# Performance work log

Hardware: AMD Instinct MI355X
Metric: run time of the kernel (lower is better)

## Reference

```python
import jax, jax.numpy as jnp
import numpy as np

ROOT_2 = 1.41421
C = 256
DIV = 4
CP = C // DIV  # 64


def _spectral_normalize(w2d):
    # exact largest singular value (torch uses power iteration approx of this)
    s = jnp.linalg.norm(w2d, ord=2)
    return w2d / s


def setup_inputs() -> dict:
    key = jax.random.key(0)
    ks = jax.random.split(key, 10)
    B, H, W = 8, 64, 64
    x = jax.random.normal(ks[0], (B, C, H, W), dtype=jnp.float32)
    # 1x1 conv weights stored as [out, in]; spectral-normalized like torch's spectral_norm
    def conv_w(k, o, i):
        w = jax.random.normal(k, (o, i), dtype=jnp.float32) * (1.0 / np.sqrt(i))
        return _spectral_normalize(w)
    Wq = conv_w(ks[1], CP, C); bq = jnp.zeros((CP,), jnp.float32)
    Wk = conv_w(ks[2], CP, C); bk = jnp.zeros((CP,), jnp.float32)
    Wv = conv_w(ks[3], CP, C); bv = jnp.zeros((CP,), jnp.float32)
    Wo = conv_w(ks[4], C, CP); bo = jnp.zeros((C,), jnp.float32)
    gamma = jnp.zeros((1,), jnp.float32)
    return {"x": x, "Wq": Wq, "bq": bq, "Wk": Wk, "bk": bk,
            "Wv": Wv, "bv": bv, "Wo": Wo, "bo": bo, "gamma": gamma}


def reference(x, Wq, bq, Wk, bk, Wv, bv, Wo, bo, gamma):
    B, c, h, w = x.shape
    n = h * w
    const1 = jnp.float32(ROOT_2 / np.sqrt(C))       # Weight_Scaling(in_channels)
    const2 = jnp.float32(ROOT_2 / np.sqrt(CP))      # Weight_Scaling(in_channels//div_num)
    xs = (const1 * x).reshape(B, c, n)              # [B,C,N]
    q = jnp.einsum('oc,bcn->bon', Wq, xs) + bq[None, :, None]  # [B,C',N]
    k = jnp.einsum('oc,bcn->bon', Wk, xs) + bk[None, :, None]
    v = jnp.einsum('oc,bcn->bon', Wv, xs) + bv[None, :, None]
    # attn[b,i,j] = softmax_j(q[:,i]^T k[:,j])
    scores = jnp.einsum('bcn,bcm->bnm', q, k)       # [B,N,N]
    attn = jax.nn.softmax(scores, axis=-1)
    sa = jnp.einsum('bcm,bnm->bcn', v, attn)        # v @ attn^T
    sa = const2 * sa
    out = jnp.einsum('oc,bcn->bon', Wo, sa) + bo[None, :, None]  # [B,C,N]
    out = out.reshape(B, c, h, w)
    return gamma[0] * out + x
```

## Files before the change

### kernel.cpp

```cpp
#include <hip/hip_runtime.h>


#define Bsz 8
#define Cch 256
#define CPd 64
#define Nn  4096
#define TIL 64
#define NSPL 4
#define MQUAR (Nn / NSPL)

typedef __attribute__((ext_vector_type(8))) short short8;
typedef __attribute__((ext_vector_type(4))) float f32x4;

static constexpr float C1 = (float)(1.41421 / 16.0);
static constexpr float C2 = (float)(1.41421 / 8.0);

__device__ inline unsigned pk_trunc(float lo, float hi) {
    return __builtin_amdgcn_perm(__float_as_uint(hi), __float_as_uint(lo), 0x07060302u);
}
__device__ inline float dpp_swap1(float v) {
    return __uint_as_float((unsigned)__builtin_amdgcn_mov_dpp(
        (int)__float_as_uint(v), 0xB1, 0xF, 0xF, true));
}
__device__ __forceinline__ void gl16(const unsigned short* g, unsigned short* s) {
    __builtin_amdgcn_global_load_lds(
        (const __attribute__((address_space(1))) void*)g,
        (__attribute__((address_space(3))) void*)s, 16, 0, 0);
}

__global__ __launch_bounds__(256) void wconv_kernel(
    const float* __restrict__ Wq, const float* __restrict__ Wk,
    const float* __restrict__ Wv, const float* __restrict__ Wo,
    unsigned short* __restrict__ Wb)
{
    const int idx = (blockIdx.x * 256 + threadIdx.x) * 4;
    const float* src = (idx < 16384) ? Wq : (idx < 32768) ? Wk : (idx < 49152) ? Wv : Wo;
    const float4 v = *(const float4*)(src + (idx & 16383));
    *(uint2*)(Wb + idx) = make_uint2(pk_trunc(v.x, v.y), pk_trunc(v.z, v.w));
}

__global__ __launch_bounds__(256) void qkv_kernel(
    const float* __restrict__ x, const unsigned short* __restrict__ Wb,
    const float* __restrict__ bq, const float* __restrict__ bk, const float* __restrict__ bv,
    unsigned short* __restrict__ qT, unsigned short* __restrict__ kT,
    unsigned short* __restrict__ vB)
{
    __shared__ __align__(16) unsigned short Wlds[CPd * 264];
    __shared__ __align__(16) float T[TIL * 68];

    const int b   = blockIdx.y;
    const int n0  = blockIdx.x * TIL;
    const int t   = threadIdx.x;
    const int g   = t >> 6;
    const int l15 = t & 15;
    const int l4  = (t & 63) >> 4;

    const float* xb = x + (size_t)b * Cch * Nn + n0 + 16 * g + l15;
    short8 xf[8];
    #pragma unroll
    for (int ks = 0; ks < 8; ++ks) {
        float xr[8];
        #pragma unroll
        for (int j = 0; j < 8; ++j)
            xr[j] = C1 * xb[(size_t)(8 * l4 + 32 * ks + j) * Nn];
        union { unsigned u[4]; short8 s; } p;
        p.u[0] = pk_trunc(xr[0], xr[1]); p.u[1] = pk_trunc(xr[2], xr[3]);
        p.u[2] = pk_trunc(xr[4], xr[5]); p.u[3] = pk_trunc(xr[6], xr[7]);
        xf[ks] = p.s;
    }

    #pragma unroll
    for (int mat = 0; mat < 3; ++mat) {
        {
            const uint4* wg = (const uint4*)(Wb + mat * 16384);
            #pragma unroll
            for (int p = 0; p < 8; ++p) {
                const int idx = p * 256 + t;
                const int o = idx >> 5, cs = idx & 31;
                *(uint4*)&Wlds[o * 264 + cs * 8] = wg[idx];
            }
        }
        __syncthreads();

        const float* bias = (mat == 0) ? bq : (mat == 1) ? bk : bv;
        f32x4 acc[4];
        #pragma unroll
        for (int st = 0; st < 4; ++st) {
            const float bb = bias[16 * st + l15];
            acc[st] = (f32x4){bb, bb, bb, bb};
        }
        #pragma unroll
        for (int st = 0; st < 4; ++st) {
            #pragma unroll
            for (int ks = 0; ks < 8; ++ks) {
                const short8 wf = *(const short8*)&Wlds[(16 * st + l15) * 264 + 8 * l4 + 32 * ks];
                acc[st] = __builtin_amdgcn_mfma_f32_16x16x32_bf16(xf[ks], wf, acc[st], 0, 0, 0);
            }
        }
        __syncthreads();

        if (mat < 2) {
            #pragma unroll
            for (int st = 0; st < 4; ++st)
                #pragma unroll
                for (int r = 0; r < 4; ++r)
                    T[(16 * g + 4 * l4 + r) * 68 + 16 * st + l15] = acc[st][r];
        } else {
            #pragma unroll
            for (int st = 0; st < 4; ++st)
                #pragma unroll
                for (int r = 0; r < 4; ++r)
                    T[(16 * st + l15) * 68 + 16 * g + 4 * l4 + r] = acc[st][r];
        }
        __syncthreads();

        const int row = t >> 2;
        const int sg  = 16 * (t & 3);
        const float4 a0 = *(const float4*)&T[row * 68 + sg + 0];
        const float4 a1 = *(const float4*)&T[row * 68 + sg + 4];
        const float4 a2 = *(const float4*)&T[row * 68 + sg + 8];
        const float4 a3 = *(const float4*)&T[row * 68 + sg + 12];
        const uint4 lo = make_uint4(pk_trunc(a0.x, a0.y), pk_trunc(a0.z, a0.w),
                                    pk_trunc(a1.x, a1.y), pk_trunc(a1.z, a1.w));
        const uint4 hi = make_uint4(pk_trunc(a2.x, a2.y), pk_trunc(a2.z, a2.w),
                                    pk_trunc(a3.x, a3.y), pk_trunc(a3.z, a3.w));
        unsigned short* dst;
        if (mat < 2) {
            dst = (mat == 0 ? qT : kT) + ((size_t)(b * Nn + n0 + row)) * CPd + sg;
        } else {
            dst = vB + ((size_t)(b * CPd + row)) * Nn + n0 + sg;
        }
        *(uint4*)dst = lo;
        *(uint4*)(dst + 8) = hi;
    }
}

__global__ __launch_bounds__(256, 6) void flash_kernel(
    const unsigned short* __restrict__ qT, const unsigned short* __restrict__ kT,
    const unsigned short* __restrict__ vB, float* __restrict__ Op, float* __restrict__ Lg)
{
    __shared__ __align__(16) unsigned short Ks[TIL * 64];
    __shared__ __align__(16) unsigned short Vs[TIL * 64];
    __shared__ __align__(16) unsigned Pb[TIL * 34];
    __shared__ float Lsh[TIL];

    const int b   = blockIdx.y;
    const int n0  = blockIdx.x * TIL;
    const int s   = blockIdx.z;
    const int t   = threadIdx.x;
    const int l   = t & 63;
    const int g   = t >> 6;
    const int l15 = l & 15;
    const int l4  = l >> 4;
    const int par = l & 1;
    const unsigned sel = par ? 0x03020706u : 0x07060302u;
    const int l15h = l15 >> 1;

    if (t < TIL) Lsh[t] = 0.f;

    const unsigned short* qp = qT + (size_t)(b * Nn + n0 + 16 * g + l15) * CPd + 8 * l4;
    const short8 qf0 = *(const short8*)qp;
    const short8 qf1 = *(const short8*)(qp + 32);

    f32x4 acco[4];
    #pragma unroll
    for (int ct = 0; ct < 4; ++ct) acco[ct] = (f32x4){0.f, 0.f, 0.f, 0.f};
    float Lp[4] = {0.f, 0.f, 0.f, 0.f};

    const int r16 = (l >> 3) & 7;
    const int sch = (l & 7) ^ r16;
    const unsigned short* kSrc = kT + (size_t)b * Nn * CPd
                               + (size_t)(16 * g + r16) * CPd + sch * 8;
    const unsigned short* vSrc = vB + (size_t)b * CPd * Nn
                               + (size_t)(16 * g + r16) * Nn + sch * 8;
    unsigned short* KsW = &Ks[(16 * g) * 64];
    unsigned short* VsW = &Vs[(16 * g) * 64];

    const int h7  = l15 & 7;
    const int sw0 = (l4 ^ h7) << 4;
    const char* KsB = (const char*)Ks + (l15 << 7);
    const char* VsB = (const char*)Vs + (l15 << 7);

    const int mbase = s * MQUAR;
    for (int mi = 0; mi < MQUAR; mi += TIL) {
        const int m0 = mbase + mi;
        __syncthreads();
        gl16(kSrc + (size_t)m0 * CPd,       KsW);
        gl16(kSrc + (size_t)(m0 + 8) * CPd, KsW + 8 * 64);
        gl16(vSrc + m0,                     VsW);
        gl16(vSrc + (size_t)8 * Nn + m0,    VsW + 8 * 64);
        __syncthreads();

        f32x4 accs[4];
        #pragma unroll
        for (int st = 0; st < 4; ++st) {
            accs[st] = (f32x4){0.f, 0.f, 0.f, 0.f};
            const short8 kf0 = *(const short8*)(KsB + (st << 11) + sw0);
            const short8 kf1 = *(const short8*)(KsB + (st << 11) + (sw0 ^ 64));
            accs[st] = __builtin_amdgcn_mfma_f32_16x16x32_bf16(qf0, kf0, accs[st], 0, 0, 0);
            accs[st] = __builtin_amdgcn_mfma_f32_16x16x32_bf16(qf1, kf1, accs[st], 0, 0, 0);
        }

        #pragma unroll
        for (int st = 0; st < 4; ++st) {
            unsigned u[4];
            #pragma unroll
            for (int r = 0; r < 4; ++r) {
                float p = __expf(accs[st][r]);
                Lp[r] += p;
                float nb = dpp_swap1(p);
                u[r] = __builtin_amdgcn_perm(__float_as_uint(nb), __float_as_uint(p), sel);
            }
            const int rb = 16 * g + 4 * l4 + 2 * par;
            Pb[(rb + 0) * 34 + 8 * st + l15h] = u[2 * par];
            Pb[(rb + 1) * 34 + 8 * st + l15h] = u[2 * par + 1];
        }
        __syncthreads();

        #pragma unroll
        for (int ks = 0; ks < 2; ++ks) {
            const short8 pf = *(const short8*)&Pb[(16 * g + l15) * 34 + 4 * l4 + 16 * ks];
            const int swk = sw0 ^ (ks << 6);
            #pragma unroll
            for (int ct = 0; ct < 4; ++ct) {
                const short8 vf = *(const short8*)(VsB + (ct << 11) + swk);
                acco[ct] = __builtin_amdgcn_mfma_f32_16x16x32_bf16(pf, vf, acco[ct], 0, 0, 0);
            }
        }
    }

    #pragma unroll
    for (int r = 0; r < 4; ++r) atomicAdd(&Lsh[16 * g + 4 * l4 + r], Lp[r]);
    __syncthreads();

    float* ob = Op + ((size_t)(b * Nn + n0)) * CPd;
    #pragma unroll
    for (int r = 0; r < 4; ++r) {
        const int nl = 16 * g + 4 * l4 + r;
        #pragma unroll
        for (int ct = 0; ct < 4; ++ct)
            atomicAdd(&ob[(size_t)nl * CPd + 16 * ct + l15], acco[ct][r]);
    }
    if (t < TIL) atomicAdd(&Lg[(size_t)b * Nn + n0 + t], Lsh[t]);
}

__global__ __launch_bounds__(512) void out_kernel(
    const float* __restrict__ Op, const float* __restrict__ Lg,
    const unsigned short* __restrict__ Wob,
    const float* __restrict__ bo, const float* __restrict__ gamma,
    const float* __restrict__ x, float* __restrict__ y)
{
    __shared__ __align__(16) unsigned short Wos[Cch * 72];
    __shared__ __align__(16) unsigned short Sas[TIL * 72];
    __shared__ float bos[Cch];

    const int b   = blockIdx.y;
    const int n0  = blockIdx.x * TIL;
    const int t   = threadIdx.x;
    const int l   = t & 63;
    const int w   = t >> 6;
    const int l15 = l & 15;
    const int l4  = l >> 4;

    if (t < Cch) bos[t] = bo[t];
    {
        const uint4* wg = (const uint4*)Wob;
        #pragma unroll
        for (int p = 0; p < 4; ++p) {
            const int idx = p * 512 + t;
            const int row = idx >> 3, seg = idx & 7;
            *(uint4*)&Wos[row * 72 + seg * 8] = wg[idx];
        }
    }
    if (t < 256) {
        const int n = t >> 2, seg = t & 3;
        const float* o0 = Op + ((size_t)(b * Nn + n0 + n)) * CPd + seg * 16;
        const float sc = C2 / Lg[(size_t)b * Nn + n0 + n];
        unsigned pk[8];
        #pragma unroll
        for (int i = 0; i < 4; ++i) {
            const float4 a = ((const float4*)o0)[i];
            pk[2 * i]     = pk_trunc(a.x * sc, a.y * sc);
            pk[2 * i + 1] = pk_trunc(a.z * sc, a.w * sc);
        }
        *(uint4*)&Sas[n * 72 + seg * 16]     = make_uint4(pk[0], pk[1], pk[2], pk[3]);
        *(uint4*)&Sas[n * 72 + seg * 16 + 8] = make_uint4(pk[4], pk[5], pk[6], pk[7]);
    }
    __syncthreads();

    short8 bfr[4][2];
    #pragma unroll
    for (int ns = 0; ns < 4; ++ns) {
        bfr[ns][0] = *(const short8*)&Sas[(16 * ns + l15) * 72 + 8 * l4];
        bfr[ns][1] = *(const short8*)&Sas[(16 * ns + l15) * 72 + 8 * l4 + 32];
    }
    const float gam = gamma[0];
    const float* xb = x + (size_t)b * Cch * Nn;
    float*       yb = y + (size_t)b * Cch * Nn;

    #pragma unroll
    for (int os2 = 0; os2 < 2; ++os2) {
        const int obase = 16 * (w + 8 * os2);
        const short8 af0 = *(const short8*)&Wos[(obase + l15) * 72 + 8 * l4];
        const short8 af1 = *(const short8*)&Wos[(obase + l15) * 72 + 8 * l4 + 32];
        #pragma unroll
        for (int ns = 0; ns < 4; ++ns) {
            f32x4 acc = (f32x4){0.f, 0.f, 0.f, 0.f};
            acc = __builtin_amdgcn_mfma_f32_16x16x32_bf16(af0, bfr[ns][0], acc, 0, 0, 0);
            acc = __builtin_amdgcn_mfma_f32_16x16x32_bf16(af1, bfr[ns][1], acc, 0, 0, 0);
            #pragma unroll
            for (int r = 0; r < 4; ++r) {
                const int o = obase + 4 * l4 + r;
                const size_t idx = (size_t)o * Nn + n0 + 16 * ns + l15;
                yb[idx] = fmaf(gam, acc[r] + bos[o], xb[idx]);
            }
        }
    }
}

extern "C" void kernel_launch(void* const* d_in, const int* in_sizes, int n_in,
                              void* d_out, int out_size, void* d_ws, size_t ws_size,
                              hipStream_t stream)
{
    (void)in_sizes; (void)n_in; (void)out_size; (void)ws_size;
    const float* x     = (const float*)d_in[0];
    const float* Wq    = (const float*)d_in[1];
    const float* bq    = (const float*)d_in[2];
    const float* Wk    = (const float*)d_in[3];
    const float* bk    = (const float*)d_in[4];
    const float* Wv    = (const float*)d_in[5];
    const float* bv    = (const float*)d_in[6];
    const float* Wo    = (const float*)d_in[7];
    const float* bo    = (const float*)d_in[8];
    const float* gamma = (const float*)d_in[9];
    float* y = (float*)d_out;

    const size_t per = (size_t)Bsz * Nn * CPd;
    unsigned short* qT = (unsigned short*)d_ws;
    unsigned short* kT = qT + per;
    unsigned short* vB = kT + per;
    float* Op = (float*)(vB + per);
    float* Lg = Op + per;
    unsigned short* Wb = (unsigned short*)(Lg + (size_t)Bsz * Nn);

    hipMemsetAsync(Op, 0, (per + (size_t)Bsz * Nn) * sizeof(float), stream);

    dim3 grid(Nn / TIL, Bsz);
    dim3 gridF(Nn / TIL, Bsz, NSPL);
    wconv_kernel<<<64, 256, 0, stream>>>(Wq, Wk, Wv, Wo, Wb);
    qkv_kernel<<<grid, 256, 0, stream>>>(x, Wb, bq, bk, bv, qT, kT, vB);
    flash_kernel<<<gridF, 256, 0, stream>>>(qT, kT, vB, Op, Lg);
    out_kernel<<<grid, 512, 0, stream>>>(Op, Lg, Wb + 3 * 16384, bo, gamma, x, y);
}
```

Baseline: 190.8 us.

## Restructure flash kernel around 32x32 MFMA with register P and double-buffered V

Rewrites the attention kernel to use 32x32x16 bf16 MFMA with a 128-query block per workgroup. K is read directly from global memory into registers instead of through LDS. The exp'd scores are repacked in registers with permlane32_swap rather than staged through an LDS buffer. V tiles are double-buffered in LDS, and the key dimension is split 8 ways instead of 4. The aim is fewer LDS round trips and barriers per tile and better MFMA efficiency. In exchange it uses more registers and lower occupancy, and performs more atomic adds to the partial outputs because of the larger split.

Measured after the change: 206.2 us. 1.08x slower.

```diff
diff --git a/kernel.cpp b/kernel.cpp
--- a/kernel.cpp
+++ b/kernel.cpp
@@ -6,21 +6,21 @@
 #define CPd 64
 #define Nn  4096
 #define TIL 64
-#define NSPL 4
+#define QBLK 128
+#define KVB 64
+#define NSPL 8
 #define MQUAR (Nn / NSPL)
 
 typedef __attribute__((ext_vector_type(8))) short short8;
 typedef __attribute__((ext_vector_type(4))) float f32x4;
+typedef __attribute__((ext_vector_type(16))) float f32x16;
+typedef __attribute__((ext_vector_type(2))) unsigned uint2v;
 
 static constexpr float C1 = (float)(1.41421 / 16.0);
 static constexpr float C2 = (float)(1.41421 / 8.0);
 
 __device__ inline unsigned pk_trunc(float lo, float hi) {
     return __builtin_amdgcn_perm(__float_as_uint(hi), __float_as_uint(lo), 0x07060302u);
-}
-__device__ inline float dpp_swap1(float v) {
-    return __uint_as_float((unsigned)__builtin_amdgcn_mov_dpp(
-        (int)__float_as_uint(v), 0xB1, 0xF, 0xF, true));
 }
 __device__ __forceinline__ void gl16(const unsigned short* g, unsigned short* s) {
     __builtin_amdgcn_global_load_lds(
@@ -135,113 +135,131 @@
     }
 }
 
-__global__ __launch_bounds__(256, 6) void flash_kernel(
+__global__ __launch_bounds__(256, 3) void flash_kernel(
     const unsigned short* __restrict__ qT, const unsigned short* __restrict__ kT,
     const unsigned short* __restrict__ vB, float* __restrict__ Op, float* __restrict__ Lg)
 {
-    __shared__ __align__(16) unsigned short Ks[TIL * 64];
-    __shared__ __align__(16) unsigned short Vs[TIL * 64];
-    __shared__ __align__(16) unsigned Pb[TIL * 34];
-    __shared__ float Lsh[TIL];
+    __shared__ __align__(16) unsigned short Vs[2][KVB * KVB];
 
     const int b   = blockIdx.y;
-    const int n0  = blockIdx.x * TIL;
+    const int n0  = blockIdx.x * QBLK;
     const int s   = blockIdx.z;
     const int t   = threadIdx.x;
     const int l   = t & 63;
     const int g   = t >> 6;
-    const int l15 = l & 15;
-    const int l4  = l >> 4;
-    const int par = l & 1;
-    const unsigned sel = par ? 0x03020706u : 0x07060302u;
-    const int l15h = l15 >> 1;
-
-    if (t < TIL) Lsh[t] = 0.f;
-
-    const unsigned short* qp = qT + (size_t)(b * Nn + n0 + 16 * g + l15) * CPd + 8 * l4;
-    const short8 qf0 = *(const short8*)qp;
-    const short8 qf1 = *(const short8*)(qp + 32);
-
-    f32x4 acco[4];
-    #pragma unroll
-    for (int ct = 0; ct < 4; ++ct) acco[ct] = (f32x4){0.f, 0.f, 0.f, 0.f};
-    float Lp[4] = {0.f, 0.f, 0.f, 0.f};
-
-    const int r16 = (l >> 3) & 7;
-    const int sch = (l & 7) ^ r16;
-    const unsigned short* kSrc = kT + (size_t)b * Nn * CPd
-                               + (size_t)(16 * g + r16) * CPd + sch * 8;
-    const unsigned short* vSrc = vB + (size_t)b * CPd * Nn
-                               + (size_t)(16 * g + r16) * Nn + sch * 8;
-    unsigned short* KsW = &Ks[(16 * g) * 64];
-    unsigned short* VsW = &Vs[(16 * g) * 64];
-
-    const int h7  = l15 & 7;
-    const int sw0 = (l4 ^ h7) << 4;
-    const char* KsB = (const char*)Ks + (l15 << 7);
-    const char* VsB = (const char*)Vs + (l15 << 7);
-
+    const int l31 = l & 31;
+    const int hi  = l >> 5;
+
+    const unsigned short* qp = qT + ((size_t)(b * Nn + n0 + 32 * g + l31)) * CPd + 8 * hi;
+    short8 qf[4];
+    #pragma unroll
+    for (int ks = 0; ks < 4; ++ks) qf[ks] = *(const short8*)(qp + 16 * ks);
+
+    const int vrow = t >> 3;
+    const unsigned short* vSrc = vB + (size_t)b * CPd * Nn + (size_t)vrow * Nn
+                               + 8 * ((t & 7) ^ (vrow & 7));
+    const unsigned short* vSrc2 = vSrc + (size_t)32 * Nn;
+
+    const unsigned short* kB = kT + (size_t)b * Nn * CPd;
     const int mbase = s * MQUAR;
-    for (int mi = 0; mi < MQUAR; mi += TIL) {
-        const int m0 = mbase + mi;
+
+    f32x16 acco[2];
+    #pragma unroll
+    for (int ch = 0; ch < 2; ++ch)
+        #pragma unroll
+        for (int i = 0; i < 16; ++i) acco[ch][i] = 0.f;
+    float Lacc = 0.f;
+
+    {
+        unsigned short* dst = &Vs[0][t * 8];
+        gl16(vSrc + mbase, dst);
+        gl16(vSrc2 + mbase, dst + 2048);
+    }
+
+    const int nt = MQUAR / KVB;
+    for (int ti = 0; ti < nt; ++ti) {
+        const int m0 = mbase + ti * KVB;
+
+        short8 kf[2][4];
+        #pragma unroll
+        for (int mh = 0; mh < 2; ++mh) {
+            const unsigned short* kp = kB + (size_t)(m0 + 32 * mh + l31) * CPd + 8 * hi;
+            #pragma unroll
+            for (int ks = 0; ks < 4; ++ks) kf[mh][ks] = *(const short8*)(kp + 16 * ks);
+        }
+
         __syncthreads();
-        gl16(kSrc + (size_t)m0 * CPd,       KsW);
-        gl16(kSrc + (size_t)(m0 + 8) * CPd, KsW + 8 * 64);
-        gl16(vSrc + m0,                     VsW);
-        gl16(vSrc + (size_t)8 * Nn + m0,    VsW + 8 * 64);
-        __syncthreads();
-
-        f32x4 accs[4];
-        #pragma unroll
-        for (int st = 0; st < 4; ++st) {
-            accs[st] = (f32x4){0.f, 0.f, 0.f, 0.f};
-            const short8 kf0 = *(const short8*)(KsB + (st << 11) + sw0);
-            const short8 kf1 = *(const short8*)(KsB + (st << 11) + (sw0 ^ 64));
-            accs[st] = __builtin_amdgcn_mfma_f32_16x16x32_bf16(qf0, kf0, accs[st], 0, 0, 0);
-            accs[st] = __builtin_amdgcn_mfma_f32_16x16x32_bf16(qf1, kf1, accs[st], 0, 0, 0);
-        }
-
-        #pragma unroll
-        for (int st = 0; st < 4; ++st) {
-            unsigned u[4];
-            #pragma unroll
-            for (int r = 0; r < 4; ++r) {
-                float p = __expf(accs[st][r]);
-                Lp[r] += p;
-                float nb = dpp_swap1(p);
-                u[r] = __builtin_amdgcn_perm(__float_as_uint(nb), __float_as_uint(p), sel);
-            }
-            const int rb = 16 * g + 4 * l4 + 2 * par;
-            Pb[(rb + 0) * 34 + 8 * st + l15h] = u[2 * par];
-            Pb[(rb + 1) * 34 + 8 * st + l15h] = u[2 * par + 1];
-        }
-        __syncthreads();
-
-        #pragma unroll
-        for (int ks = 0; ks < 2; ++ks) {
-            const short8 pf = *(const short8*)&Pb[(16 * g + l15) * 34 + 4 * l4 + 16 * ks];
-            const int swk = sw0 ^ (ks << 6);
-            #pragma unroll
-            for (int ct = 0; ct < 4; ++ct) {
-                const short8 vf = *(const short8*)(VsB + (ct << 11) + swk);
-                acco[ct] = __builtin_amdgcn_mfma_f32_16x16x32_bf16(pf, vf, acco[ct], 0, 0, 0);
-            }
-        }
-    }
-
-    #pragma unroll
-    for (int r = 0; r < 4; ++r) atomicAdd(&Lsh[16 * g + 4 * l4 + r], Lp[r]);
-    __syncthreads();
-
-    float* ob = Op + ((size_t)(b * Nn + n0)) * CPd;
-    #pragma unroll
-    for (int r = 0; r < 4; ++r) {
-        const int nl = 16 * g + 4 * l4 + r;
-        #pragma unroll
-        for (int ct = 0; ct < 4; ++ct)
-            atomicAdd(&ob[(size_t)nl * CPd + 16 * ct + l15], acco[ct][r]);
-    }
-    if (t < TIL) atomicAdd(&Lg[(size_t)b * Nn + n0 + t], Lsh[t]);
+
+        if (ti + 1 < nt) {
+            unsigned short* dst = &Vs[(ti + 1) & 1][t * 8];
+            gl16(vSrc + m0 + KVB, dst);
+            gl16(vSrc2 + m0 + KVB, dst + 2048);
+        }
+
+        f32x16 accs[2];
+        #pragma unroll
+        for (int mh = 0; mh < 2; ++mh) {
+            #pragma unroll
+            for (int i = 0; i < 16; ++i) accs[mh][i] = 0.f;
+            #pragma unroll
+            for (int ks = 0; ks < 4; ++ks)
+                accs[mh] = __builtin_amdgcn_mfma_f32_32x32x16_bf16(kf[mh][ks], qf[ks],
+                                                                   accs[mh], 0, 0, 0);
+        }
+
+        short8 pa[4];
+        #pragma unroll
+        for (int mh = 0; mh < 2; ++mh) {
+            float p[16];
+            #pragma unroll
+            for (int r = 0; r < 16; ++r) {
+                p[r] = __expf(accs[mh][r]);
+                Lacc += p[r];
+            }
+            unsigned uA[4], uB[4];
+            #pragma unroll
+            for (int q = 0; q < 4; ++q) {
+                uA[q] = pk_trunc(p[4 * q + 0], p[4 * q + 1]);
+                uB[q] = pk_trunc(p[4 * q + 2], p[4 * q + 3]);
+            }
+            #pragma unroll
+            for (int k2 = 0; k2 < 2; ++k2) {
+                uint2v wa = __builtin_amdgcn_permlane32_swap(uA[2 * k2], uA[2 * k2 + 1],
+                                                             false, false);
+                uint2v wb = __builtin_amdgcn_permlane32_swap(uB[2 * k2], uB[2 * k2 + 1],
+                                                             false, false);
+                union { unsigned u[4]; short8 s; } w;
+                w.u[0] = wa[0]; w.u[1] = wb[0]; w.u[2] = wa[1]; w.u[3] = wb[1];
+                pa[2 * mh + k2] = w.s;
+            }
+        }
+
+        const unsigned short* Vr = Vs[ti & 1];
+        #pragma unroll
+        for (int ks = 0; ks < 4; ++ks) {
+            #pragma unroll
+            for (int ch = 0; ch < 2; ++ch) {
+                const int row  = 32 * ch + l31;
+                const int phys = (2 * ks + hi) ^ (l & 7);
+                const short8 vf = *(const short8*)&Vr[row * KVB + 8 * phys];
+                acco[ch] = __builtin_amdgcn_mfma_f32_32x32x16_bf16(pa[ks], vf,
+                                                                   acco[ch], 0, 0, 0);
+            }
+        }
+    }
+
+    const float Ltot = Lacc + __shfl_xor(Lacc, 32, 64);
+    if (hi == 0)
+        atomicAdd(&Lg[(size_t)b * Nn + n0 + 32 * g + l31], Ltot);
+
+    float* ob = Op + ((size_t)(b * Nn + n0 + 32 * g)) * CPd;
+    #pragma unroll
+    for (int r = 0; r < 16; ++r) {
+        const int nl = (r & 3) + 8 * (r >> 2) + 4 * hi;
+        #pragma unroll
+        for (int ch = 0; ch < 2; ++ch)
+            atomicAdd(&ob[(size_t)nl * CPd + 32 * ch + l31], acco[ch][r]);
+    }
 }
 
 __global__ __launch_bounds__(512) void out_kernel(
@@ -346,7 +364,7 @@
     hipMemsetAsync(Op, 0, (per + (size_t)Bsz * Nn) * sizeof(float), stream);
 
     dim3 grid(Nn / TIL, Bsz);
-    dim3 gridF(Nn / TIL, Bsz, NSPL);
+    dim3 gridF(Nn / QBLK, Bsz, NSPL);
     wconv_kernel<<<64, 256, 0, stream>>>(Wq, Wk, Wv, Wo, Wb);
     qkv_kernel<<<grid, 256, 0, stream>>>(x, Wb, bq, bk, bv, qT, kT, vB);
     flash_kernel<<<gridF, 256, 0, stream>>>(qT, kT, vB, Op, Lg);
```

## Split qkv and output projections across more waves and blocks

Applied to the files above, without the earlier changes.

The qkv kernel now runs 512 threads per block, with each wave handling half the output channels, so twice as many waves share the same x tile. The x fragment loads are duplicated across the two halves. The output kernel splits the 256 output channels over two blocks via a z-grid dimension, halving per-block LDS and registers to raise occupancy. In exchange the normalized attention output Op is read and converted twice, once per split block.

Measured after the change: 197.6 us. +3.5%, slower.

```diff
diff --git a/kernel.cpp b/kernel.cpp
--- a/kernel.cpp
+++ b/kernel.cpp
@@ -39,7 +39,7 @@
     *(uint2*)(Wb + idx) = make_uint2(pk_trunc(v.x, v.y), pk_trunc(v.z, v.w));
 }
 
-__global__ __launch_bounds__(256) void qkv_kernel(
+__global__ __launch_bounds__(512, 4) void qkv_kernel(
     const float* __restrict__ x, const unsigned short* __restrict__ Wb,
     const float* __restrict__ bq, const float* __restrict__ bk, const float* __restrict__ bv,
     unsigned short* __restrict__ qT, unsigned short* __restrict__ kT,
@@ -52,10 +52,12 @@
     const int n0  = blockIdx.x * TIL;
     const int t   = threadIdx.x;
     const int g   = t >> 6;
+    const int ns_ = g & 3;
+    const int oh  = g >> 2;
     const int l15 = t & 15;
     const int l4  = (t & 63) >> 4;
 
-    const float* xb = x + (size_t)b * Cch * Nn + n0 + 16 * g + l15;
+    const float* xb = x + (size_t)b * Cch * Nn + n0 + 16 * ns_ + l15;
     short8 xf[8];
     #pragma unroll
     for (int ks = 0; ks < 8; ++ks) {
@@ -74,8 +76,8 @@
         {
             const uint4* wg = (const uint4*)(Wb + mat * 16384);
             #pragma unroll
-            for (int p = 0; p < 8; ++p) {
-                const int idx = p * 256 + t;
+            for (int p = 0; p < 4; ++p) {
+                const int idx = p * 512 + t;
                 const int o = idx >> 5, cs = idx & 31;
                 *(uint4*)&Wlds[o * 264 + cs * 8] = wg[idx];
             }
@@ -83,55 +85,51 @@
         __syncthreads();
 
         const float* bias = (mat == 0) ? bq : (mat == 1) ? bk : bv;
-        f32x4 acc[4];
-        #pragma unroll
-        for (int st = 0; st < 4; ++st) {
-            const float bb = bias[16 * st + l15];
-            acc[st] = (f32x4){bb, bb, bb, bb};
-        }
-        #pragma unroll
-        for (int st = 0; st < 4; ++st) {
+        f32x4 acc[2];
+        #pragma unroll
+        for (int i = 0; i < 2; ++i) {
+            const float bb = bias[16 * (2 * oh + i) + l15];
+            acc[i] = (f32x4){bb, bb, bb, bb};
+        }
+        #pragma unroll
+        for (int i = 0; i < 2; ++i) {
+            const int st = 2 * oh + i;
             #pragma unroll
             for (int ks = 0; ks < 8; ++ks) {
                 const short8 wf = *(const short8*)&Wlds[(16 * st + l15) * 264 + 8 * l4 + 32 * ks];
-                acc[st] = __builtin_amdgcn_mfma_f32_16x16x32_bf16(xf[ks], wf, acc[st], 0, 0, 0);
+                acc[i] = __builtin_amdgcn_mfma_f32_16x16x32_bf16(xf[ks], wf, acc[i], 0, 0, 0);
             }
         }
         __syncthreads();
 
         if (mat < 2) {
             #pragma unroll
-            for (int st = 0; st < 4; ++st)
+            for (int i = 0; i < 2; ++i)
                 #pragma unroll
                 for (int r = 0; r < 4; ++r)
-                    T[(16 * g + 4 * l4 + r) * 68 + 16 * st + l15] = acc[st][r];
+                    T[(16 * ns_ + 4 * l4 + r) * 68 + 16 * (2 * oh + i) + l15] = acc[i][r];
         } else {
             #pragma unroll
-            for (int st = 0; st < 4; ++st)
+            for (int i = 0; i < 2; ++i)
                 #pragma unroll
                 for (int r = 0; r < 4; ++r)
-                    T[(16 * st + l15) * 68 + 16 * g + 4 * l4 + r] = acc[st][r];
-        }
-        __syncthreads();
-
-        const int row = t >> 2;
-        const int sg  = 16 * (t & 3);
+                    T[(16 * (2 * oh + i) + l15) * 68 + 16 * ns_ + 4 * l4 + r] = acc[i][r];
+        }
+        __syncthreads();
+
+        const int row = t >> 3;
+        const int sg  = 8 * (t & 7);
         const float4 a0 = *(const float4*)&T[row * 68 + sg + 0];
         const float4 a1 = *(const float4*)&T[row * 68 + sg + 4];
-        const float4 a2 = *(const float4*)&T[row * 68 + sg + 8];
-        const float4 a3 = *(const float4*)&T[row * 68 + sg + 12];
-        const uint4 lo = make_uint4(pk_trunc(a0.x, a0.y), pk_trunc(a0.z, a0.w),
+        const uint4 o4 = make_uint4(pk_trunc(a0.x, a0.y), pk_trunc(a0.z, a0.w),
                                     pk_trunc(a1.x, a1.y), pk_trunc(a1.z, a1.w));
-        const uint4 hi = make_uint4(pk_trunc(a2.x, a2.y), pk_trunc(a2.z, a2.w),
-                                    pk_trunc(a3.x, a3.y), pk_trunc(a3.z, a3.w));
         unsigned short* dst;
         if (mat < 2) {
             dst = (mat == 0 ? qT : kT) + ((size_t)(b * Nn + n0 + row)) * CPd + sg;
         } else {
             dst = vB + ((size_t)(b * CPd + row)) * Nn + n0 + sg;
         }
-        *(uint4*)dst = lo;
-        *(uint4*)(dst + 8) = hi;
+        *(uint4*)dst = o4;
     }
 }
 
@@ -244,29 +242,30 @@
     if (t < TIL) atomicAdd(&Lg[(size_t)b * Nn + n0 + t], Lsh[t]);
 }
 
-__global__ __launch_bounds__(512) void out_kernel(
+__global__ __launch_bounds__(512, 8) void out_kernel(
     const float* __restrict__ Op, const float* __restrict__ Lg,
     const unsigned short* __restrict__ Wob,
     const float* __restrict__ bo, const float* __restrict__ gamma,
     const float* __restrict__ x, float* __restrict__ y)
 {
-    __shared__ __align__(16) unsigned short Wos[Cch * 72];
+    __shared__ __align__(16) unsigned short Wos[128 * 72];
     __shared__ __align__(16) unsigned short Sas[TIL * 72];
-    __shared__ float bos[Cch];
+    __shared__ float bos[128];
 
     const int b   = blockIdx.y;
     const int n0  = blockIdx.x * TIL;
+    const int oz  = blockIdx.z;
     const int t   = threadIdx.x;
     const int l   = t & 63;
     const int w   = t >> 6;
     const int l15 = l & 15;
     const int l4  = l >> 4;
 
-    if (t < Cch) bos[t] = bo[t];
+    if (t < 128) bos[t] = bo[128 * oz + t];
     {
-        const uint4* wg = (const uint4*)Wob;
-        #pragma unroll
-        for (int p = 0; p < 4; ++p) {
+        const uint4* wg = (const uint4*)Wob + 1024 * oz;
+        #pragma unroll
+        for (int p = 0; p < 2; ++p) {
             const int idx = p * 512 + t;
             const int row = idx >> 3, seg = idx & 7;
             *(uint4*)&Wos[row * 72 + seg * 8] = wg[idx];
@@ -288,32 +287,25 @@
     }
     __syncthreads();
 
-    short8 bfr[4][2];
+    const float gam = gamma[0];
+    const float* xb = x + (size_t)(b * Cch + 128 * oz) * Nn;
+    float*       yb = y + (size_t)(b * Cch + 128 * oz) * Nn;
+
+    const int obase = 16 * w;
+    const short8 af0 = *(const short8*)&Wos[(obase + l15) * 72 + 8 * l4];
+    const short8 af1 = *(const short8*)&Wos[(obase + l15) * 72 + 8 * l4 + 32];
     #pragma unroll
     for (int ns = 0; ns < 4; ++ns) {
-        bfr[ns][0] = *(const short8*)&Sas[(16 * ns + l15) * 72 + 8 * l4];
-        bfr[ns][1] = *(const short8*)&Sas[(16 * ns + l15) * 72 + 8 * l4 + 32];
-    }
-    const float gam = gamma[0];
-    const float* xb = x + (size_t)b * Cch * Nn;
-    float*       yb = y + (size_t)b * Cch * Nn;
-
-    #pragma unroll
-    for (int os2 = 0; os2 < 2; ++os2) {
-        const int obase = 16 * (w + 8 * os2);
-        const short8 af0 = *(const short8*)&Wos[(obase + l15) * 72 + 8 * l4];
-        const short8 af1 = *(const short8*)&Wos[(obase + l15) * 72 + 8 * l4 + 32];
-        #pragma unroll
-        for (int ns = 0; ns < 4; ++ns) {
-            f32x4 acc = (f32x4){0.f, 0.f, 0.f, 0.f};
-            acc = __builtin_amdgcn_mfma_f32_16x16x32_bf16(af0, bfr[ns][0], acc, 0, 0, 0);
-            acc = __builtin_amdgcn_mfma_f32_16x16x32_bf16(af1, bfr[ns][1], acc, 0, 0, 0);
-            #pragma unroll
-            for (int r = 0; r < 4; ++r) {
-                const int o = obase + 4 * l4 + r;
-                const size_t idx = (size_t)o * Nn + n0 + 16 * ns + l15;
-                yb[idx] = fmaf(gam, acc[r] + bos[o], xb[idx]);
-            }
+        const short8 b0 = *(const short8*)&Sas[(16 * ns + l15) * 72 + 8 * l4];
+        const short8 b1 = *(const short8*)&Sas[(16 * ns + l15) * 72 + 8 * l4 + 32];
+        f32x4 acc = (f32x4){0.f, 0.f, 0.f, 0.f};
+        acc = __builtin_amdgcn_mfma_f32_16x16x32_bf16(af0, b0, acc, 0, 0, 0);
+        acc = __builtin_amdgcn_mfma_f32_16x16x32_bf16(af1, b1, acc, 0, 0, 0);
+        #pragma unroll
+        for (int r = 0; r < 4; ++r) {
+            const int ol = obase + 4 * l4 + r;
+            const size_t idx = (size_t)ol * Nn + n0 + 16 * ns + l15;
+            yb[idx] = fmaf(gam, acc[r] + bos[ol], xb[idx]);
         }
     }
 }
@@ -346,9 +338,10 @@
     hipMemsetAsync(Op, 0, (per + (size_t)Bsz * Nn) * sizeof(float), stream);
 
     dim3 grid(Nn / TIL, Bsz);
+    dim3 gridO(Nn / TIL, Bsz, 2);
     dim3 gridF(Nn / TIL, Bsz, NSPL);
     wconv_kernel<<<64, 256, 0, stream>>>(Wq, Wk, Wv, Wo, Wb);
-    qkv_kernel<<<grid, 256, 0, stream>>>(x, Wb, bq, bk, bv, qT, kT, vB);
+    qkv_kernel<<<grid, 512, 0, stream>>>(x, Wb, bq, bk, bv, qT, kT, vB);
     flash_kernel<<<gridF, 256, 0, stream>>>(qT, kT, vB, Op, Lg);
-    out_kernel<<<grid, 512, 0, stream>>>(Op, Lg, Wb + 3 * 16384, bo, gamma, x, y);
-}
+    out_kernel<<<gridO, 512, 0, stream>>>(Op, Lg, Wb + 3 * 16384, bo, gamma, x, y);
+}
```

## Double-buffer K/V tiles in flash kernel with 128-row query blocks

Applied to the files above, without the earlier changes.

The flash kernel now runs 512 threads over 128 query rows per block and ping-pongs two K/V LDS buffers. The next tile's global-to-LDS load is issued while the current tile is computed, which drops one barrier per tile. Log2(e) is folded into Wq and bq so the softmax can use exp2f in place of __expf. Row sums are reduced with wave shuffles and written straight to global atomics instead of going through shared-memory atomics. The risks are that the P buffer write/read inside COMPUTE now has no barrier between waves, and that the larger blocks may lower occupancy.

Result: no change. 190.6 us (-0.1%).

```diff
diff --git a/kernel.cpp b/kernel.cpp
--- a/kernel.cpp
+++ b/kernel.cpp
@@ -6,6 +6,7 @@
 #define CPd 64
 #define Nn  4096
 #define TIL 64
+#define QROWS 128
 #define NSPL 4
 #define MQUAR (Nn / NSPL)
 
@@ -14,6 +15,7 @@
 
 static constexpr float C1 = (float)(1.41421 / 16.0);
 static constexpr float C2 = (float)(1.41421 / 8.0);
+static constexpr float LOG2E = 1.44269504f;
 
 __device__ inline unsigned pk_trunc(float lo, float hi) {
     return __builtin_amdgcn_perm(__float_as_uint(hi), __float_as_uint(lo), 0x07060302u);
@@ -35,8 +37,10 @@
 {
     const int idx = (blockIdx.x * 256 + threadIdx.x) * 4;
     const float* src = (idx < 16384) ? Wq : (idx < 32768) ? Wk : (idx < 49152) ? Wv : Wo;
+    const float sc = (idx < 16384) ? LOG2E : 1.0f;
     const float4 v = *(const float4*)(src + (idx & 16383));
-    *(uint2*)(Wb + idx) = make_uint2(pk_trunc(v.x, v.y), pk_trunc(v.z, v.w));
+    *(uint2*)(Wb + idx) = make_uint2(pk_trunc(sc * v.x, sc * v.y),
+                                     pk_trunc(sc * v.z, sc * v.w));
 }
 
 __global__ __launch_bounds__(256) void qkv_kernel(
@@ -83,10 +87,11 @@
         __syncthreads();
 
         const float* bias = (mat == 0) ? bq : (mat == 1) ? bk : bv;
+        const float bsc = (mat == 0) ? LOG2E : 1.0f;
         f32x4 acc[4];
         #pragma unroll
         for (int st = 0; st < 4; ++st) {
-            const float bb = bias[16 * st + l15];
+            const float bb = bsc * bias[16 * st + l15];
             acc[st] = (f32x4){bb, bb, bb, bb};
         }
         #pragma unroll
@@ -135,30 +140,29 @@
     }
 }
 
-__global__ __launch_bounds__(256, 6) void flash_kernel(
+__global__ __launch_bounds__(512, 6) void flash_kernel(
     const unsigned short* __restrict__ qT, const unsigned short* __restrict__ kT,
     const unsigned short* __restrict__ vB, float* __restrict__ Op, float* __restrict__ Lg)
 {
-    __shared__ __align__(16) unsigned short Ks[TIL * 64];
-    __shared__ __align__(16) unsigned short Vs[TIL * 64];
-    __shared__ __align__(16) unsigned Pb[TIL * 34];
-    __shared__ float Lsh[TIL];
+    __shared__ __align__(16) unsigned short Ks0[TIL * 64];
+    __shared__ __align__(16) unsigned short Ks1[TIL * 64];
+    __shared__ __align__(16) unsigned short Vs0[TIL * 64];
+    __shared__ __align__(16) unsigned short Vs1[TIL * 64];
+    __shared__ __align__(16) unsigned Pb[QROWS * 34];
 
     const int b   = blockIdx.y;
-    const int n0  = blockIdx.x * TIL;
+    const int n0  = blockIdx.x * QROWS;
     const int s   = blockIdx.z;
     const int t   = threadIdx.x;
     const int l   = t & 63;
-    const int g   = t >> 6;
+    const int w   = t >> 6;
     const int l15 = l & 15;
     const int l4  = l >> 4;
     const int par = l & 1;
     const unsigned sel = par ? 0x03020706u : 0x07060302u;
     const int l15h = l15 >> 1;
 
-    if (t < TIL) Lsh[t] = 0.f;
-
-    const unsigned short* qp = qT + (size_t)(b * Nn + n0 + 16 * g + l15) * CPd + 8 * l4;
+    const unsigned short* qp = qT + (size_t)(b * Nn + n0 + 16 * w + l15) * CPd + 8 * l4;
     const short8 qf0 = *(const short8*)qp;
     const short8 qf1 = *(const short8*)(qp + 32);
 
@@ -167,30 +171,27 @@
     for (int ct = 0; ct < 4; ++ct) acco[ct] = (f32x4){0.f, 0.f, 0.f, 0.f};
     float Lp[4] = {0.f, 0.f, 0.f, 0.f};
 
-    const int r16 = (l >> 3) & 7;
-    const int sch = (l & 7) ^ r16;
-    const unsigned short* kSrc = kT + (size_t)b * Nn * CPd
-                               + (size_t)(16 * g + r16) * CPd + sch * 8;
-    const unsigned short* vSrc = vB + (size_t)b * CPd * Nn
-                               + (size_t)(16 * g + r16) * Nn + sch * 8;
-    unsigned short* KsW = &Ks[(16 * g) * 64];
-    unsigned short* VsW = &Vs[(16 * g) * 64];
+    const int r8  = l >> 3;
+    const int sch = (l & 7) ^ r8;
+    const unsigned short* kPtr = kT + (size_t)b * Nn * CPd
+                               + (size_t)(8 * w + r8) * CPd + 8 * sch;
+    const unsigned short* vPtr = vB + (size_t)b * CPd * Nn
+                               + (size_t)(8 * w + r8) * Nn + 8 * sch;
+    const int ldsOff = 8 * w * 64;
 
     const int h7  = l15 & 7;
     const int sw0 = (l4 ^ h7) << 4;
-    const char* KsB = (const char*)Ks + (l15 << 7);
-    const char* VsB = (const char*)Vs + (l15 << 7);
 
     const int mbase = s * MQUAR;
-    for (int mi = 0; mi < MQUAR; mi += TIL) {
-        const int m0 = mbase + mi;
-        __syncthreads();
-        gl16(kSrc + (size_t)m0 * CPd,       KsW);
-        gl16(kSrc + (size_t)(m0 + 8) * CPd, KsW + 8 * 64);
-        gl16(vSrc + m0,                     VsW);
-        gl16(vSrc + (size_t)8 * Nn + m0,    VsW + 8 * 64);
-        __syncthreads();
-
+    const int nt = MQUAR / TIL;
+
+    auto STAGE = [&](unsigned short* KD, unsigned short* VD, int m0) {
+        gl16(kPtr + (size_t)m0 * CPd, KD + ldsOff);
+        gl16(vPtr + m0,               VD + ldsOff);
+    };
+    auto COMPUTE = [&](const unsigned short* Kb, const unsigned short* Vb) {
+        const char* KsB = (const char*)Kb + (l15 << 7);
+        const char* VsB = (const char*)Vb + (l15 << 7);
         f32x4 accs[4];
         #pragma unroll
         for (int st = 0; st < 4; ++st) {
@@ -200,26 +201,23 @@
             accs[st] = __builtin_amdgcn_mfma_f32_16x16x32_bf16(qf0, kf0, accs[st], 0, 0, 0);
             accs[st] = __builtin_amdgcn_mfma_f32_16x16x32_bf16(qf1, kf1, accs[st], 0, 0, 0);
         }
-
         #pragma unroll
         for (int st = 0; st < 4; ++st) {
             unsigned u[4];
             #pragma unroll
             for (int r = 0; r < 4; ++r) {
-                float p = __expf(accs[st][r]);
+                float p = exp2f(accs[st][r]);
                 Lp[r] += p;
                 float nb = dpp_swap1(p);
                 u[r] = __builtin_amdgcn_perm(__float_as_uint(nb), __float_as_uint(p), sel);
             }
-            const int rb = 16 * g + 4 * l4 + 2 * par;
+            const int rb = 16 * w + 4 * l4 + 2 * par;
             Pb[(rb + 0) * 34 + 8 * st + l15h] = u[2 * par];
             Pb[(rb + 1) * 34 + 8 * st + l15h] = u[2 * par + 1];
         }
-        __syncthreads();
-
         #pragma unroll
         for (int ks = 0; ks < 2; ++ks) {
-            const short8 pf = *(const short8*)&Pb[(16 * g + l15) * 34 + 4 * l4 + 16 * ks];
+            const short8 pf = *(const short8*)&Pb[(16 * w + l15) * 34 + 4 * l4 + 16 * ks];
             const int swk = sw0 ^ (ks << 6);
             #pragma unroll
             for (int ct = 0; ct < 4; ++ct) {
@@ -227,21 +225,40 @@
                 acco[ct] = __builtin_amdgcn_mfma_f32_16x16x32_bf16(pf, vf, acco[ct], 0, 0, 0);
             }
         }
-    }
-
-    #pragma unroll
-    for (int r = 0; r < 4; ++r) atomicAdd(&Lsh[16 * g + 4 * l4 + r], Lp[r]);
+    };
+
+    STAGE(Ks0, Vs0, mbase);
     __syncthreads();
-
-    float* ob = Op + ((size_t)(b * Nn + n0)) * CPd;
+    for (int ti = 0; ti < nt; ti += 2) {
+        const int m0 = mbase + ti * TIL;
+        STAGE(Ks1, Vs1, m0 + TIL);
+        COMPUTE(Ks0, Vs0);
+        __syncthreads();
+        if (ti + 2 < nt) STAGE(Ks0, Vs0, m0 + 2 * TIL);
+        COMPUTE(Ks1, Vs1);
+        __syncthreads();
+    }
+
     #pragma unroll
     for (int r = 0; r < 4; ++r) {
-        const int nl = 16 * g + 4 * l4 + r;
+        float v = Lp[r];
+        v += __shfl_xor(v, 1, 64); v += __shfl_xor(v, 2, 64);
+        v += __shfl_xor(v, 4, 64); v += __shfl_xor(v, 8, 64);
+        Lp[r] = v;
+    }
+    if (l15 == 0) {
+        #pragma unroll
+        for (int r = 0; r < 4; ++r)
+            atomicAdd(&Lg[(size_t)b * Nn + n0 + 16 * w + 4 * l4 + r], Lp[r]);
+    }
+    float* ob = Op + ((size_t)(b * Nn + n0 + 16 * w)) * CPd;
+    #pragma unroll
+    for (int r = 0; r < 4; ++r) {
+        const int nl = 4 * l4 + r;
         #pragma unroll
         for (int ct = 0; ct < 4; ++ct)
             atomicAdd(&ob[(size_t)nl * CPd + 16 * ct + l15], acco[ct][r]);
     }
-    if (t < TIL) atomicAdd(&Lg[(size_t)b * Nn + n0 + t], Lsh[t]);
 }
 
 __global__ __launch_bounds__(512) void out_kernel(
@@ -346,9 +363,9 @@
     hipMemsetAsync(Op, 0, (per + (size_t)Bsz * Nn) * sizeof(float), stream);
 
     dim3 grid(Nn / TIL, Bsz);
-    dim3 gridF(Nn / TIL, Bsz, NSPL);
+    dim3 gridF(Nn / QROWS, Bsz, NSPL);
     wconv_kernel<<<64, 256, 0, stream>>>(Wq, Wk, Wv, Wo, Wb);
     qkv_kernel<<<grid, 256, 0, stream>>>(x, Wb, bq, bk, bv, qT, kT, vB);
-    flash_kernel<<<gridF, 256, 0, stream>>>(qT, kT, vB, Op, Lg);
+    flash_kernel<<<gridF, 512, 0, stream>>>(qT, kT, vB, Op, Lg);
     out_kernel<<<grid, 512, 0, stream>>>(Op, Lg, Wb + 3 * 16384, bo, gamma, x, y);
 }
```
